# Kernel optimization log

Measured on AMD Instinct MI355X. Metric: run time of the kernel, lower is better.

Reference implementation:

```python
import jax, jax.numpy as jnp
import numpy as np

RADIUS = 1.0
BUMP = 32          # config.bump_steps
SCALE = 100.0      # sigmoid sharpness in compute_ecc
G = 32             # num_graphs

N, E, F = 16000, 48000, 32000
DIM, NDIR = 3, 64
HID, NC = 256, 10


def compute_ecc(h, index, lin):
    # h: [M, D]; lin: [BUMP] thresholds; index: [M] graph ids
    # sigmoid(scale * (lin - h)) broadcast -> [M, BUMP, D], segment-sum over M
    ecc = jax.nn.sigmoid(SCALE * (lin[None, :, None] - h[:, None, :]))
    return jax.ops.segment_sum(ecc, index, num_segments=G)  # [G, BUMP, D]


def setup_inputs() -> dict:
    key = jax.random.key(0)
    ks = jax.random.split(key, 12)
    x = jax.random.normal(ks[0], (N, DIM), dtype=jnp.float32)
    node_weights = jax.random.uniform(ks[1], (N,), dtype=jnp.float32)
    edge_weights = jax.random.uniform(ks[2], (E,), dtype=jnp.float32)
    face_weights = jax.random.uniform(ks[3], (F,), dtype=jnp.float32)
    v = jax.random.normal(ks[4], (DIM, NDIR), dtype=jnp.float32)
    v = v / jnp.linalg.norm(v, axis=0, keepdims=True)  # unit directions
    W1 = jax.random.normal(ks[5], (HID, NDIR * BUMP), dtype=jnp.float32) * 0.02
    b1 = jnp.zeros((HID,), dtype=jnp.float32)
    W2 = jax.random.normal(ks[6], (NC, HID), dtype=jnp.float32) * 0.02
    b2 = jnp.zeros((NC,), dtype=jnp.float32)
    edge_index = jax.random.randint(ks[7], (2, E), 0, N, dtype=jnp.int64)
    face = jax.random.randint(ks[8], (3, F), 0, N, dtype=jnp.int64)
    batch_ids = jnp.sort(jax.random.randint(ks[9], (N,), 0, G, dtype=jnp.int64))
    return {"x": x, "node_weights": node_weights, "edge_weights": edge_weights,
            "face_weights": face_weights, "v": v, "W1": W1, "b1": b1,
            "W2": W2, "b2": b2, "edge_index": edge_index, "face": face,
            "batch_ids": batch_ids}


def reference(x, node_weights, edge_weights, face_weights, v, W1, b1, W2, b2,
              edge_index, face, batch_ids):
    lin = jnp.linspace(-RADIUS, RADIUS, BUMP, dtype=jnp.float32)
    # node heights: weighted coords projected onto directions -> [N, D]
    nh = (x * node_weights[:, None]) @ v
    # edge heights: max over the 2 endpoints, then weight -> [E, D]
    eh = jnp.maximum(nh[edge_index[0]], nh[edge_index[1]]) * edge_weights[:, None]
    idx_e = batch_ids[edge_index[0]]
    # face heights: max over the 3 vertices -> [F, D]
    fh = jnp.max(nh[face], axis=0) * face_weights[:, None]
    idx_f = batch_ids[face[0]]
    ecc = compute_ecc(nh, batch_ids, lin)   # [G, BUMP, D]
    ecc = ecc - compute_ecc(eh, idx_e, lin)
    ecc = ecc + compute_ecc(fh, idx_f, lin)
    flat = ecc.reshape(G, -1)               # [G, BUMP*D]
    h = jax.nn.relu(flat @ W1.T + b1)
    logits = h @ W2.T + b2
    return (logits, flat)
```

## Files before the change

### kernel.cpp

```cpp
#include <hip/hip_runtime.h>
#include <hip/hip_bf16.h>

constexpr int NN = 16000, NE = 48000, NF = 32000;
constexpr int ND = 64, NB = 32, NG = 32;
constexpr int HIDN = 256, NCLS = 10;
constexpr int CHB = 32;
constexpr int EFB = (NE + NF + 255) / 256;
constexpr int PREB = (NN * 16) / 256;
constexpr int CAPE = 4096, CAPF = 4096;
constexpr float KLOG = 144.26950408889634f;
constexpr float DLT  = 9.307710457348151f;
constexpr float INV_DLT = 0.10743849569269015f;
constexpr int HBINS = 39;

struct alignas(8)  ERec { unsigned ab; float w; };
struct alignas(16) FRec { unsigned ab; unsigned c; float w; unsigned pad; };

constexpr int NH_OFF   = 0;
constexpr int ECCF_OFF = NH_OFF + NN * ND;
constexpr int CUR_OFF  = ECCF_OFF + NG * NB * ND;
constexpr int NOFS_OFF = CUR_OFF + 64;
constexpr int DONE_OFF = NOFS_OFF + 40;
constexpr int ER_OFF   = DONE_OFF + 32;
constexpr int FR_OFF   = ER_OFF + NG * CAPE * 2;
constexpr int HB_OFF   = FR_OFF + NG * CAPF * 4;
constexpr int ZERO_CNT = NG * NB * ND;

__device__ __forceinline__ int clamp_node(int n) {
    return ((unsigned)n < (unsigned)NN) ? n : 0;
}
template<bool BF> __device__ __forceinline__ float ldf(const void* p, int i) {
    return BF ? __bfloat162float(((const __hip_bfloat16*)p)[i]) : ((const float*)p)[i];
}
template<bool BF> __device__ __forceinline__ float4 ldf4(const void* p, int i) {
    if (BF) {
        uint2 u = *(const uint2*)((const unsigned short*)p + i);
        float4 r;
        r.x = __uint_as_float((u.x & 0xffffu) << 16);
        r.y = __uint_as_float(u.x & 0xffff0000u);
        r.z = __uint_as_float((u.y & 0xffffu) << 16);
        r.w = __uint_as_float(u.y & 0xffff0000u);
        return r;
    }
    return *(const float4*)((const float*)p + i);
}
template<bool I64> __device__ __forceinline__ int ldi(const int* p, int i) {
    return I64 ? p[2 * i] : p[i];
}

__device__ __forceinline__ bool detect_bf(const void* xp) {
    const unsigned* xw = (const unsigned*)xp;
    unsigned w = xw[threadIdx.x & 63];
    return __ballot(((w >> 23) & 0xFFu) >= 200u) != 0ull;
}
__device__ __forceinline__ bool detect_i64(const int* eip) {
    const unsigned* eiw = (const unsigned*)eip;
    unsigned o = eiw[2 * (threadIdx.x & 63) + 1];
    return __ballot(o != 0u) == 0ull;
}

__device__ __forceinline__ void accum_hist(float h, float s, float* hb) {
    const float KDEC = __builtin_amdgcn_exp2f(-DLT);
    float hkL = fmaf(h, KLOG, KLOG);
    float fl = floorf((hkL - 14.0f) * INV_DLT);
    int jlo = (int)fl + 1;
    if (jlo >= 32) return;
    if (jlo < -4) { hb[4 * 64] += s; return; }
    float t0 = fmaf(-(fl + 1.0f), DLT, hkL);
    float e  = __builtin_amdgcn_exp2f(t0);
    float s0 = __builtin_amdgcn_rcpf(1.0f + e);  e *= KDEC;
    float s1 = __builtin_amdgcn_rcpf(1.0f + e);  e *= KDEC;
    float s2 = __builtin_amdgcn_rcpf(1.0f + e);
    float* p = hb + (jlo + 4) * 64;
    float v0 = p[0], v1 = p[64], v2 = p[128], v3 = p[192];
    p[0]   = v0 + s * s0;
    p[64]  = v1 + s * (s1 - s0);
    p[128] = v2 + s * (s2 - s1);
    p[192] = v3 + s * (1.0f - s2);
}

template<bool BF, bool I64>
__device__ __forceinline__ void pre_body(const void* x, const void* nw, const void* v,
                                         const int* ei, const int* fc, const int* batch,
                                         const void* ew, const void* fw,
                                         float* wsf, int* wsi, unsigned* cur,
                                         ERec* er, FRec* fr,
                                         unsigned* cnt, unsigned* base) {
    int t = threadIdx.x;
    int gid = blockIdx.x * 256 + t;

    if (gid < ZERO_CNT / 4) {
        float4 z; z.x = z.y = z.z = z.w = 0.0f;
        *(float4*)(wsf + ECCF_OFF + gid * 4) = z;
    }

    if (blockIdx.x == PREB - 1 && t < 32)
        ((unsigned*)wsi)[DONE_OFF + t] = 0u;

    if (gid < NN) {
        int gn = ldi<I64>(batch, gid) & (NG - 1);
        int gp = (gid > 0) ? (ldi<I64>(batch, gid - 1) & (NG - 1)) : -1;
        for (int gg = gp + 1; gg <= gn; gg++) wsi[NOFS_OFF + gg] = gid;
        if (gid == NN - 1)
            for (int gg = gn + 1; gg <= NG; gg++) wsi[NOFS_OFF + gg] = NN;
    }

    {
        int n = gid >> 4, d0 = (gid & 15) * 4;
        float x0 = ldf<BF>(x, n * 3 + 0), x1 = ldf<BF>(x, n * 3 + 1);
        float x2 = ldf<BF>(x, n * 3 + 2), wn = ldf<BF>(nw, n);
        float4 v0 = ldf4<BF>(v, d0);
        float4 v1 = ldf4<BF>(v, ND + d0);
        float4 v2 = ldf4<BF>(v, 2 * ND + d0);
        float4 h;
        h.x = fmaf(x2, v2.x, fmaf(x1, v1.x, x0 * v0.x)) * wn;
        h.y = fmaf(x2, v2.y, fmaf(x1, v1.y, x0 * v0.y)) * wn;
        h.z = fmaf(x2, v2.z, fmaf(x1, v1.z, x0 * v0.z)) * wn;
        h.w = fmaf(x2, v2.w, fmaf(x1, v1.w, x0 * v0.w)) * wn;
        *(float4*)(wsf + NH_OFF + n * ND + d0) = h;
    }

    if (blockIdx.x < EFB) {
        if (t < 64) cnt[t] = 0;
        __syncthreads();
        int id = blockIdx.x * 256 + t;
        int bin = 0; unsigned rank = 0; bool act = false;
        if (id < NE + NF) {
            if (id < NE) bin = ldi<I64>(batch, clamp_node(ldi<I64>(ei, id))) & 31;
            else bin = 32 + (ldi<I64>(batch, clamp_node(ldi<I64>(fc, id - NE))) & 31);
            act = true;
            rank = atomicAdd(&cnt[bin], 1u);
        }
        __syncthreads();
        if (t < 64) base[t] = cnt[t] ? atomicAdd(&cur[t], cnt[t]) : 0u;
        __syncthreads();
        if (act) {
            int off = (int)(base[bin] + rank);
            if (bin < 32) {
                if (off < CAPE) {
                    unsigned a = (unsigned)clamp_node(ldi<I64>(ei, id));
                    unsigned b = (unsigned)clamp_node(ldi<I64>(ei, NE + id));
                    ERec r; r.ab = a | (b << 14); r.w = ldf<BF>(ew, id);
                    er[bin * CAPE + off] = r;
                }
            } else {
                if (off < CAPF) {
                    int fid = id - NE;
                    unsigned a = (unsigned)clamp_node(ldi<I64>(fc, fid));
                    unsigned b = (unsigned)clamp_node(ldi<I64>(fc, NF + fid));
                    unsigned c = (unsigned)clamp_node(ldi<I64>(fc, 2 * NF + fid));
                    FRec r; r.ab = a | (b << 14); r.c = c;
                    r.w = ldf<BF>(fw, fid); r.pad = 0u;
                    fr[(bin - 32) * CAPF + off] = r;
                }
            }
        }
    }
}
__global__ __launch_bounds__(256) void k_pre(const void* __restrict__ x,
                                             const void* __restrict__ nw,
                                             const void* __restrict__ v,
                                             const int* __restrict__ ei,
                                             const int* __restrict__ fc,
                                             const int* __restrict__ batch,
                                             const void* __restrict__ ew,
                                             const void* __restrict__ fw,
                                             float* __restrict__ wsf,
                                             int* __restrict__ wsi,
                                             unsigned* __restrict__ cur,
                                             ERec* __restrict__ er,
                                             FRec* __restrict__ fr) {
    __shared__ unsigned cnt[64], base[64];
    bool bf = detect_bf(x), i64 = detect_i64(ei);
    if (bf)  { if (i64) pre_body<true,true >(x,nw,v,ei,fc,batch,ew,fw,wsf,wsi,cur,er,fr,cnt,base);
               else     pre_body<true,false>(x,nw,v,ei,fc,batch,ew,fw,wsf,wsi,cur,er,fr,cnt,base); }
    else     { if (i64) pre_body<false,true >(x,nw,v,ei,fc,batch,ew,fw,wsf,wsi,cur,er,fr,cnt,base);
               else     pre_body<false,false>(x,nw,v,ei,fc,batch,ew,fw,wsf,wsi,cur,er,fr,cnt,base); }
}

__global__ __launch_bounds__(256, 4) void k_ecc(const float* __restrict__ nh,
                                                const int* __restrict__ wsi,
                                                const unsigned* __restrict__ cur,
                                                float* __restrict__ eccf,
                                                const ERec* __restrict__ er,
                                                const FRec* __restrict__ fr) {
    __shared__ float hist[4 * HBINS * 64];
    int t = threadIdx.x;
    int d = t & 63;
    int w = __builtin_amdgcn_readfirstlane(t) >> 6;
    int g  = blockIdx.x >> 5;
    int cb = blockIdx.x & (CHB - 1);
    int sid = cb * 4 + w;
    const int S = CHB * 4;

    for (int j = t; j < 4 * HBINS * 64; j += 256) hist[j] = 0.0f;
    __syncthreads();

    float* hb = hist + w * (HBINS * 64) + d;

    int ns = wsi[NOFS_OFF + g], nend = wsi[NOFS_OFF + g + 1];
    int i = ns + sid;
    for (; i + 3 * S < nend; i += 4 * S) {
        float h1 = nh[i * ND + d];
        float h2 = nh[(i + S) * ND + d];
        float h3 = nh[(i + 2 * S) * ND + d];
        float h4 = nh[(i + 3 * S) * ND + d];
        accum_hist(h1, 1.0f, hb);
        accum_hist(h2, 1.0f, hb);
        accum_hist(h3, 1.0f, hb);
        accum_hist(h4, 1.0f, hb);
    }
    for (; i < nend; i += S) accum_hist(nh[i * ND + d], 1.0f, hb);

    int ecnt = min((int)cur[g], CAPE);
    const ERec* eg = er + g * CAPE;
    i = sid;
    if (i + 3 * S < ecnt) {
        ERec r1 = eg[i], r2 = eg[i + S], r3 = eg[i + 2 * S], r4 = eg[i + 3 * S];
        for (;;) {
            int ni = i + 4 * S;
            bool more = (ni + 3 * S < ecnt);
            float a1 = nh[(r1.ab & 16383) * ND + d], b1 = nh[((r1.ab >> 14) & 16383) * ND + d];
            float a2 = nh[(r2.ab & 16383) * ND + d], b2 = nh[((r2.ab >> 14) & 16383) * ND + d];
            float a3 = nh[(r3.ab & 16383) * ND + d], b3 = nh[((r3.ab >> 14) & 16383) * ND + d];
            float a4 = nh[(r4.ab & 16383) * ND + d], b4 = nh[((r4.ab >> 14) & 16383) * ND + d];
            ERec n1, n2, n3, n4;
            if (more) { n1 = eg[ni]; n2 = eg[ni + S]; n3 = eg[ni + 2 * S]; n4 = eg[ni + 3 * S]; }
            accum_hist(fmaxf(a1, b1) * r1.w, -1.0f, hb);
            accum_hist(fmaxf(a2, b2) * r2.w, -1.0f, hb);
            accum_hist(fmaxf(a3, b3) * r3.w, -1.0f, hb);
            accum_hist(fmaxf(a4, b4) * r4.w, -1.0f, hb);
            i = ni;
            if (!more) break;
            r1 = n1; r2 = n2; r3 = n3; r4 = n4;
        }
    }
    for (; i < ecnt; i += S) {
        ERec r = eg[i];
        float ha = nh[(r.ab & 16383) * ND + d], hbv = nh[((r.ab >> 14) & 16383) * ND + d];
        accum_hist(fmaxf(ha, hbv) * r.w, -1.0f, hb);
    }

    int fcnt = min((int)cur[32 + g], CAPF);
    const FRec* fg = fr + g * CAPF;
    i = sid;
    if (i + 3 * S < fcnt) {
        FRec r1 = fg[i], r2 = fg[i + S], r3 = fg[i + 2 * S], r4 = fg[i + 3 * S];
        for (;;) {
            int ni = i + 4 * S;
            bool more = (ni + 3 * S < fcnt);
            float a1 = nh[(r1.ab & 16383) * ND + d], b1 = nh[((r1.ab >> 14) & 16383) * ND + d];
            float c1 = nh[r1.c * ND + d];
            float a2 = nh[(r2.ab & 16383) * ND + d], b2 = nh[((r2.ab >> 14) & 16383) * ND + d];
            float c2 = nh[r2.c * ND + d];
            float a3 = nh[(r3.ab & 16383) * ND + d], b3 = nh[((r3.ab >> 14) & 16383) * ND + d];
            float c3 = nh[r3.c * ND + d];
            float a4 = nh[(r4.ab & 16383) * ND + d], b4 = nh[((r4.ab >> 14) & 16383) * ND + d];
            float c4 = nh[r4.c * ND + d];
            FRec n1, n2, n3, n4;
            if (more) { n1 = fg[ni]; n2 = fg[ni + S]; n3 = fg[ni + 2 * S]; n4 = fg[ni + 3 * S]; }
            accum_hist(fmaxf(fmaxf(a1, b1), c1) * r1.w, 1.0f, hb);
            accum_hist(fmaxf(fmaxf(a2, b2), c2) * r2.w, 1.0f, hb);
            accum_hist(fmaxf(fmaxf(a3, b3), c3) * r3.w, 1.0f, hb);
            accum_hist(fmaxf(fmaxf(a4, b4), c4) * r4.w, 1.0f, hb);
            i = ni;
            if (!more) break;
            r1 = n1; r2 = n2; r3 = n3; r4 = n4;
        }
    }
    for (; i < fcnt; i += S) {
        FRec r = fg[i];
        float ha = nh[(r.ab & 16383) * ND + d], hbv = nh[((r.ab >> 14) & 16383) * ND + d];
        float hc = nh[r.c * ND + d];
        accum_hist(fmaxf(fmaxf(ha, hbv), hc) * r.w, 1.0f, hb);
    }

    __syncthreads();
    for (int o = t; o < HBINS * 64; o += 256)
        hist[o] += hist[HBINS*64 + o] + hist[2*HBINS*64 + o] + hist[3*HBINS*64 + o];
    __syncthreads();
    {
        float* segw = hist + HBINS * 64;
        float run = 0.0f, pre[8];
#pragma unroll
        for (int jj = 0; jj < 8; jj++) {
            run += hist[(4 + w * 8 + jj) * 64 + d];
            pre[jj] = run;
        }
        float padb = hist[d] + hist[64 + d] + hist[128 + d] + hist[192 + d];
        segw[w * 64 + d] = run;
        __syncthreads();
        float base = padb;
#pragma unroll
        for (int u = 0; u < 3; u++) if (u < w) base += segw[u * 64 + d];
        float* eb = eccf + g * (NB * ND) + d;
#pragma unroll
        for (int jj = 0; jj < 8; jj++)
            unsafeAtomicAdd(eb + (w * 8 + jj) * 64, base + pre[jj]);
    }
}

template<bool BF>
__device__ __forceinline__ void mlp_body(const void* W1, const void* b1,
                                         const void* W2, const void* b2,
                                         const float* eccf, float* hbuf,
                                         unsigned* done, void* outv,
                                         float* red, float* pr, unsigned* lastflag) {
    int g = blockIdx.x >> 3, hc = blockIdx.x & 7;
    int t = threadIdx.x;

    const float4* fp = (const float4*)(eccf + g * (NB * ND) + t * 8);
    float4 fa = fp[0], fb = fp[1];
    float fl[8] = {fa.x, fa.y, fa.z, fa.w, fb.x, fb.y, fb.z, fb.w};

    if (hc == 0) {
        int ob = NG * NCLS + g * (NB * ND) + t * 8;
        if (BF) {
#pragma unroll
            for (int j = 0; j < 8; j++)
                ((__hip_bfloat16*)outv)[ob + j] = __float2bfloat16(fl[j]);
        } else {
            ((float4*)((float*)outv + ob))[0] = fa;
            ((float4*)((float*)outv + ob))[1] = fb;
        }
    }

    float acc[32];
#pragma unroll
    for (int r = 0; r < 32; r++) acc[r] = 0.0f;
#pragma unroll 4
    for (int r = 0; r < 32; r++) {
        size_t wb = (size_t)(hc * 32 + r) * (NB * ND) + t * 8;
        float wv[8];
        if (BF) {
            uint4 u = *(const uint4*)((const __hip_bfloat16*)W1 + wb);
            wv[0] = __uint_as_float(u.x << 16); wv[1] = __uint_as_float(u.x & 0xffff0000u);
            wv[2] = __uint_as_float(u.y << 16); wv[3] = __uint_as_float(u.y & 0xffff0000u);
            wv[4] = __uint_as_float(u.z << 16); wv[5] = __uint_as_float(u.z & 0xffff0000u);
            wv[6] = __uint_as_float(u.w << 16); wv[7] = __uint_as_float(u.w & 0xffff0000u);
        } else {
            float4 a = *(const float4*)((const float*)W1 + wb);
            float4 b = *(const float4*)((const float*)W1 + wb + 4);
            wv[0]=a.x; wv[1]=a.y; wv[2]=a.z; wv[3]=a.w;
            wv[4]=b.x; wv[5]=b.y; wv[6]=b.z; wv[7]=b.w;
        }
        float s = 0.0f;
#pragma unroll
        for (int j = 0; j < 8; j++) s = fmaf(wv[j], fl[j], s);
        acc[r] = s;
    }

#pragma unroll
    for (int r = 0; r < 32; r++) red[t * 33 + r] = acc[r];
    __syncthreads();
    {
        int r = t >> 3, s8 = t & 7;
        float sum = 0.0f;
#pragma unroll
        for (int i = 0; i < 32; i++) sum += red[(s8 * 32 + i) * 33 + r];
        pr[r * 8 + s8] = sum;
    }
    __syncthreads();
    if (t < 32) {
        float h = ldf<BF>(b1, hc * 32 + t);
#pragma unroll
        for (int s8 = 0; s8 < 8; s8++) h += pr[t * 8 + s8];
        __hip_atomic_store(&hbuf[g * HIDN + hc * 32 + t], fmaxf(h, 0.0f),
                           __ATOMIC_RELAXED, __HIP_MEMORY_SCOPE_AGENT);
    }

    __syncthreads();
    if (t == 0) {
        unsigned prev = __hip_atomic_fetch_add(&done[g], 1u, __ATOMIC_RELAXED,
                                               __HIP_MEMORY_SCOPE_AGENT);
        *lastflag = (prev == 7u) ? 1u : 0u;
    }
    __syncthreads();
    if (*lastflag) {
        red[t] = __hip_atomic_load(&hbuf[g * HIDN + t], __ATOMIC_RELAXED,
                                   __HIP_MEMORY_SCOPE_AGENT);
        __syncthreads();
        int w = t >> 6, lane = t & 63;
        for (int c = w; c < NCLS; c += 4) {
            float p = red[lane]        * ldf<BF>(W2, c * HIDN + lane)
                    + red[lane + 64]   * ldf<BF>(W2, c * HIDN + lane + 64)
                    + red[lane + 128]  * ldf<BF>(W2, c * HIDN + lane + 128)
                    + red[lane + 192]  * ldf<BF>(W2, c * HIDN + lane + 192);
#pragma unroll
            for (int off = 32; off >= 1; off >>= 1) p += __shfl_xor(p, off);
            if (lane == 0) {
                float r = p + ldf<BF>(b2, c);
                if (BF) ((__hip_bfloat16*)outv)[g * NCLS + c] = __float2bfloat16(r);
                else    ((float*)outv)[g * NCLS + c] = r;
            }
        }
    }
}
__global__ __launch_bounds__(256) void k_mlp(const void* __restrict__ W1,
                                             const void* __restrict__ b1,
                                             const void* __restrict__ W2,
                                             const void* __restrict__ b2,
                                             const float* __restrict__ eccf,
                                             float* __restrict__ hbuf,
                                             unsigned* __restrict__ done,
                                             void* __restrict__ outv,
                                             const void* __restrict__ x) {
    __shared__ float red[256 * 33];
    __shared__ float pr[256];
    __shared__ unsigned lastflag;
    if (detect_bf(x)) mlp_body<true >(W1, b1, W2, b2, eccf, hbuf, done, outv, red, pr, &lastflag);
    else              mlp_body<false>(W1, b1, W2, b2, eccf, hbuf, done, outv, red, pr, &lastflag);
}

extern "C" void kernel_launch(void* const* d_in, const int* in_sizes, int n_in,
                              void* d_out, int out_size, void* d_ws, size_t ws_size,
                              hipStream_t stream) {
    const void* x  = d_in[0];
    const void* nw = d_in[1];
    const void* ew = d_in[2];
    const void* fw = d_in[3];
    const void* v  = d_in[4];
    const void* W1 = d_in[5];
    const void* b1 = d_in[6];
    const void* W2 = d_in[7];
    const void* b2 = d_in[8];
    const int* ei    = (const int*)d_in[9];
    const int* fc    = (const int*)d_in[10];
    const int* batch = (const int*)d_in[11];

    float*    wsf = (float*)d_ws;
    unsigned* wsu = (unsigned*)d_ws;
    int*      wsi = (int*)d_ws;
    float*    nh   = wsf + NH_OFF;
    float*    eccf = wsf + ECCF_OFF;
    unsigned* cur  = wsu + CUR_OFF;
    unsigned* done = wsu + DONE_OFF;
    float*    hbuf = wsf + HB_OFF;
    ERec*     er   = (ERec*)(wsf + ER_OFF);
    FRec*     fr   = (FRec*)(wsf + FR_OFF);

    hipMemsetAsync((char*)d_ws + (size_t)CUR_OFF * 4, 0, 64 * 4, stream);

    k_pre<<<PREB, 256, 0, stream>>>(x, nw, v, ei, fc, batch, ew, fw, wsf, wsi, cur, er, fr);
    k_ecc<<<NG * CHB, 256, 0, stream>>>(nh, wsi, cur, eccf, er, fr);
    k_mlp<<<NG * 8, 256, 0, stream>>>(W1, b1, W2, b2, eccf, hbuf, done, d_out, x);
}
```

Baseline: 120.9 us.

## Drop node-height buffer; prebake weighted vertex coords into edge/face records

Stops materialising the N×64 node-height array in the pre kernel. Edge and face records now carry the pre-weighted 3D coordinates of each endpoint plus the element weight, and the ecc kernel computes heights on the fly as a dot product with the direction vector held in registers. Node heights are likewise recomputed from x and the node weights. This replaces the scattered per-direction gathers from the 4 MB height buffer with contiguous float4 record loads. The cost is larger records (32 or 48 bytes each), more FMAs in the histogram loop, and a shallower unroll with no software prefetch.

```diff
diff --git a/kernel.cpp b/kernel.cpp
--- a/kernel.cpp
+++ b/kernel.cpp
@@ -6,24 +6,20 @@
 constexpr int HIDN = 256, NCLS = 10;
 constexpr int CHB = 32;
 constexpr int EFB = (NE + NF + 255) / 256;
-constexpr int PREB = (NN * 16) / 256;
+constexpr int PREB = EFB;
 constexpr int CAPE = 4096, CAPF = 4096;
 constexpr float KLOG = 144.26950408889634f;
 constexpr float DLT  = 9.307710457348151f;
 constexpr float INV_DLT = 0.10743849569269015f;
 constexpr int HBINS = 39;
 
-struct alignas(8)  ERec { unsigned ab; float w; };
-struct alignas(16) FRec { unsigned ab; unsigned c; float w; unsigned pad; };
-
-constexpr int NH_OFF   = 0;
-constexpr int ECCF_OFF = NH_OFF + NN * ND;
+constexpr int ECCF_OFF = 0;
 constexpr int CUR_OFF  = ECCF_OFF + NG * NB * ND;
 constexpr int NOFS_OFF = CUR_OFF + 64;
 constexpr int DONE_OFF = NOFS_OFF + 40;
 constexpr int ER_OFF   = DONE_OFF + 32;
-constexpr int FR_OFF   = ER_OFF + NG * CAPE * 2;
-constexpr int HB_OFF   = FR_OFF + NG * CAPF * 4;
+constexpr int FR_OFF   = ER_OFF + NG * CAPE * 8;
+constexpr int HB_OFF   = FR_OFF + NG * CAPF * 12;
 constexpr int ZERO_CNT = NG * NB * ND;
 
 __device__ __forceinline__ int clamp_node(int n) {
@@ -31,18 +27,6 @@
 }
 template<bool BF> __device__ __forceinline__ float ldf(const void* p, int i) {
     return BF ? __bfloat162float(((const __hip_bfloat16*)p)[i]) : ((const float*)p)[i];
-}
-template<bool BF> __device__ __forceinline__ float4 ldf4(const void* p, int i) {
-    if (BF) {
-        uint2 u = *(const uint2*)((const unsigned short*)p + i);
-        float4 r;
-        r.x = __uint_as_float((u.x & 0xffffu) << 16);
-        r.y = __uint_as_float(u.x & 0xffff0000u);
-        r.z = __uint_as_float((u.y & 0xffffu) << 16);
-        r.w = __uint_as_float(u.y & 0xffff0000u);
-        return r;
-    }
-    return *(const float4*)((const float*)p + i);
 }
 template<bool I64> __device__ __forceinline__ int ldi(const int* p, int i) {
     return I64 ? p[2 * i] : p[i];
@@ -57,6 +41,10 @@
     const unsigned* eiw = (const unsigned*)eip;
     unsigned o = eiw[2 * (threadIdx.x & 63) + 1];
     return __ballot(o != 0u) == 0ull;
+}
+
+__device__ __forceinline__ float dot3w(float4 p, float v0, float v1, float v2) {
+    return fmaf(p.z, v2, fmaf(p.y, v1, p.x * v0));
 }
 
 __device__ __forceinline__ void accum_hist(float h, float s, float* hb) {
@@ -80,11 +68,11 @@
 }
 
 template<bool BF, bool I64>
-__device__ __forceinline__ void pre_body(const void* x, const void* nw, const void* v,
+__device__ __forceinline__ void pre_body(const void* x, const void* nw,
                                          const int* ei, const int* fc, const int* batch,
                                          const void* ew, const void* fw,
                                          float* wsf, int* wsi, unsigned* cur,
-                                         ERec* er, FRec* fr,
+                                         float4* er4, float4* fr4,
                                          unsigned* cnt, unsigned* base) {
     int t = threadIdx.x;
     int gid = blockIdx.x * 256 + t;
@@ -94,7 +82,7 @@
         *(float4*)(wsf + ECCF_OFF + gid * 4) = z;
     }
 
-    if (blockIdx.x == PREB - 1 && t < 32)
+    if (blockIdx.x == 0 && t < 32)
         ((unsigned*)wsi)[DONE_OFF + t] = 0u;
 
     if (gid < NN) {
@@ -106,24 +94,9 @@
     }
 
     {
-        int n = gid >> 4, d0 = (gid & 15) * 4;
-        float x0 = ldf<BF>(x, n * 3 + 0), x1 = ldf<BF>(x, n * 3 + 1);
-        float x2 = ldf<BF>(x, n * 3 + 2), wn = ldf<BF>(nw, n);
-        float4 v0 = ldf4<BF>(v, d0);
-        float4 v1 = ldf4<BF>(v, ND + d0);
-        float4 v2 = ldf4<BF>(v, 2 * ND + d0);
-        float4 h;
-        h.x = fmaf(x2, v2.x, fmaf(x1, v1.x, x0 * v0.x)) * wn;
-        h.y = fmaf(x2, v2.y, fmaf(x1, v1.y, x0 * v0.y)) * wn;
-        h.z = fmaf(x2, v2.z, fmaf(x1, v1.z, x0 * v0.z)) * wn;
-        h.w = fmaf(x2, v2.w, fmaf(x1, v1.w, x0 * v0.w)) * wn;
-        *(float4*)(wsf + NH_OFF + n * ND + d0) = h;
-    }
-
-    if (blockIdx.x < EFB) {
         if (t < 64) cnt[t] = 0;
         __syncthreads();
-        int id = blockIdx.x * 256 + t;
+        int id = gid;
         int bin = 0; unsigned rank = 0; bool act = false;
         if (id < NE + NF) {
             if (id < NE) bin = ldi<I64>(batch, clamp_node(ldi<I64>(ei, id))) & 31;
@@ -138,20 +111,43 @@
             int off = (int)(base[bin] + rank);
             if (bin < 32) {
                 if (off < CAPE) {
-                    unsigned a = (unsigned)clamp_node(ldi<I64>(ei, id));
-                    unsigned b = (unsigned)clamp_node(ldi<I64>(ei, NE + id));
-                    ERec r; r.ab = a | (b << 14); r.w = ldf<BF>(ew, id);
-                    er[bin * CAPE + off] = r;
+                    int a = clamp_node(ldi<I64>(ei, id));
+                    int b = clamp_node(ldi<I64>(ei, NE + id));
+                    float wa = ldf<BF>(nw, a), wb = ldf<BF>(nw, b);
+                    float4 ra, rb;
+                    ra.x = ldf<BF>(x, 3*a)   * wa;
+                    ra.y = ldf<BF>(x, 3*a+1) * wa;
+                    ra.z = ldf<BF>(x, 3*a+2) * wa;
+                    ra.w = ldf<BF>(ew, id);
+                    rb.x = ldf<BF>(x, 3*b)   * wb;
+                    rb.y = ldf<BF>(x, 3*b+1) * wb;
+                    rb.z = ldf<BF>(x, 3*b+2) * wb;
+                    rb.w = 0.0f;
+                    float4* dst = er4 + ((size_t)bin * CAPE + off) * 2;
+                    dst[0] = ra; dst[1] = rb;
                 }
             } else {
                 if (off < CAPF) {
                     int fid = id - NE;
-                    unsigned a = (unsigned)clamp_node(ldi<I64>(fc, fid));
-                    unsigned b = (unsigned)clamp_node(ldi<I64>(fc, NF + fid));
-                    unsigned c = (unsigned)clamp_node(ldi<I64>(fc, 2 * NF + fid));
-                    FRec r; r.ab = a | (b << 14); r.c = c;
-                    r.w = ldf<BF>(fw, fid); r.pad = 0u;
-                    fr[(bin - 32) * CAPF + off] = r;
+                    int a = clamp_node(ldi<I64>(fc, fid));
+                    int b = clamp_node(ldi<I64>(fc, NF + fid));
+                    int c = clamp_node(ldi<I64>(fc, 2 * NF + fid));
+                    float wa = ldf<BF>(nw, a), wb = ldf<BF>(nw, b), wc = ldf<BF>(nw, c);
+                    float4 qa, qb, qc;
+                    qa.x = ldf<BF>(x, 3*a)   * wa;
+                    qa.y = ldf<BF>(x, 3*a+1) * wa;
+                    qa.z = ldf<BF>(x, 3*a+2) * wa;
+                    qa.w = ldf<BF>(fw, fid);
+                    qb.x = ldf<BF>(x, 3*b)   * wb;
+                    qb.y = ldf<BF>(x, 3*b+1) * wb;
+                    qb.z = ldf<BF>(x, 3*b+2) * wb;
+                    qb.w = 0.0f;
+                    qc.x = ldf<BF>(x, 3*c)   * wc;
+                    qc.y = ldf<BF>(x, 3*c+1) * wc;
+                    qc.z = ldf<BF>(x, 3*c+2) * wc;
+                    qc.w = 0.0f;
+                    float4* dst = fr4 + ((size_t)(bin - 32) * CAPF + off) * 3;
+                    dst[0] = qa; dst[1] = qb; dst[2] = qc;
                 }
             }
         }
@@ -159,7 +155,6 @@
 }
 __global__ __launch_bounds__(256) void k_pre(const void* __restrict__ x,
                                              const void* __restrict__ nw,
-                                             const void* __restrict__ v,
                                              const int* __restrict__ ei,
                                              const int* __restrict__ fc,
                                              const int* __restrict__ batch,
@@ -168,23 +163,21 @@
                                              float* __restrict__ wsf,
                                              int* __restrict__ wsi,
                                              unsigned* __restrict__ cur,
-                                             ERec* __restrict__ er,
-                                             FRec* __restrict__ fr) {
+                                             float4* __restrict__ er4,
+                                             float4* __restrict__ fr4) {
     __shared__ unsigned cnt[64], base[64];
     bool bf = detect_bf(x), i64 = detect_i64(ei);
-    if (bf)  { if (i64) pre_body<true,true >(x,nw,v,ei,fc,batch,ew,fw,wsf,wsi,cur,er,fr,cnt,base);
-               else     pre_body<true,false>(x,nw,v,ei,fc,batch,ew,fw,wsf,wsi,cur,er,fr,cnt,base); }
-    else     { if (i64) pre_body<false,true >(x,nw,v,ei,fc,batch,ew,fw,wsf,wsi,cur,er,fr,cnt,base);
-               else     pre_body<false,false>(x,nw,v,ei,fc,batch,ew,fw,wsf,wsi,cur,er,fr,cnt,base); }
-}
-
-__global__ __launch_bounds__(256, 4) void k_ecc(const float* __restrict__ nh,
-                                                const int* __restrict__ wsi,
-                                                const unsigned* __restrict__ cur,
-                                                float* __restrict__ eccf,
-                                                const ERec* __restrict__ er,
-                                                const FRec* __restrict__ fr) {
-    __shared__ float hist[4 * HBINS * 64];
+    if (bf)  { if (i64) pre_body<true,true >(x,nw,ei,fc,batch,ew,fw,wsf,wsi,cur,er4,fr4,cnt,base);
+               else     pre_body<true,false>(x,nw,ei,fc,batch,ew,fw,wsf,wsi,cur,er4,fr4,cnt,base); }
+    else     { if (i64) pre_body<false,true >(x,nw,ei,fc,batch,ew,fw,wsf,wsi,cur,er4,fr4,cnt,base);
+               else     pre_body<false,false>(x,nw,ei,fc,batch,ew,fw,wsf,wsi,cur,er4,fr4,cnt,base); }
+}
+
+template<bool BF>
+__device__ __forceinline__ void ecc_body(const void* xx, const void* nw, const void* vv,
+                                         const int* wsi, const unsigned* cur,
+                                         float* eccf, const float4* er4,
+                                         const float4* fr4, float* hist) {
     int t = threadIdx.x;
     int d = t & 63;
     int w = __builtin_amdgcn_readfirstlane(t) >> 6;
@@ -193,91 +186,76 @@
     int sid = cb * 4 + w;
     const int S = CHB * 4;
 
-    for (int j = t; j < 4 * HBINS * 64; j += 256) hist[j] = 0.0f;
+    float v0 = ldf<BF>(vv, d), v1 = ldf<BF>(vv, ND + d), v2 = ldf<BF>(vv, 2 * ND + d);
+
+    float4* h4 = (float4*)hist;
+    const int Q = HBINS * 16;
+    float4 z; z.x = z.y = z.z = z.w = 0.0f;
+    for (int j = t; j < 4 * Q; j += 256) h4[j] = z;
     __syncthreads();
 
     float* hb = hist + w * (HBINS * 64) + d;
 
     int ns = wsi[NOFS_OFF + g], nend = wsi[NOFS_OFF + g + 1];
     int i = ns + sid;
-    for (; i + 3 * S < nend; i += 4 * S) {
-        float h1 = nh[i * ND + d];
-        float h2 = nh[(i + S) * ND + d];
-        float h3 = nh[(i + 2 * S) * ND + d];
-        float h4 = nh[(i + 3 * S) * ND + d];
+    for (; i + S < nend; i += 2 * S) {
+        int j = i + S;
+        float a0 = ldf<BF>(xx, 3*i), a1 = ldf<BF>(xx, 3*i+1), a2 = ldf<BF>(xx, 3*i+2);
+        float wa = ldf<BF>(nw, i);
+        float b0 = ldf<BF>(xx, 3*j), b1 = ldf<BF>(xx, 3*j+1), b2 = ldf<BF>(xx, 3*j+2);
+        float wb = ldf<BF>(nw, j);
+        accum_hist(fmaf(a2, v2, fmaf(a1, v1, a0 * v0)) * wa, 1.0f, hb);
+        accum_hist(fmaf(b2, v2, fmaf(b1, v1, b0 * v0)) * wb, 1.0f, hb);
+    }
+    for (; i < nend; i += S) {
+        float a0 = ldf<BF>(xx, 3*i), a1 = ldf<BF>(xx, 3*i+1), a2 = ldf<BF>(xx, 3*i+2);
+        float wa = ldf<BF>(nw, i);
+        accum_hist(fmaf(a2, v2, fmaf(a1, v1, a0 * v0)) * wa, 1.0f, hb);
+    }
+
+    int ecnt = min((int)cur[g], CAPE);
+    const float4* eg = er4 + (size_t)g * CAPE * 2;
+    i = sid;
+    for (; i + S < ecnt; i += 2 * S) {
+        float4 pa1 = eg[2*i],       pb1 = eg[2*i + 1];
+        float4 pa2 = eg[2*(i+S)],   pb2 = eg[2*(i+S) + 1];
+        float h1 = fmaxf(dot3w(pa1, v0, v1, v2), dot3w(pb1, v0, v1, v2)) * pa1.w;
+        float h2 = fmaxf(dot3w(pa2, v0, v1, v2), dot3w(pb2, v0, v1, v2)) * pa2.w;
+        accum_hist(h1, -1.0f, hb);
+        accum_hist(h2, -1.0f, hb);
+    }
+    for (; i < ecnt; i += S) {
+        float4 pa = eg[2*i], pb = eg[2*i + 1];
+        accum_hist(fmaxf(dot3w(pa, v0, v1, v2), dot3w(pb, v0, v1, v2)) * pa.w,
+                   -1.0f, hb);
+    }
+
+    int fcnt = min((int)cur[32 + g], CAPF);
+    const float4* fg = fr4 + (size_t)g * CAPF * 3;
+    i = sid;
+    for (; i + S < fcnt; i += 2 * S) {
+        float4 qa1 = fg[3*i], qb1 = fg[3*i + 1], qc1 = fg[3*i + 2];
+        float4 qa2 = fg[3*(i+S)], qb2 = fg[3*(i+S) + 1], qc2 = fg[3*(i+S) + 2];
+        float h1 = fmaxf(fmaxf(dot3w(qa1, v0, v1, v2), dot3w(qb1, v0, v1, v2)),
+                         dot3w(qc1, v0, v1, v2)) * qa1.w;
+        float h2 = fmaxf(fmaxf(dot3w(qa2, v0, v1, v2), dot3w(qb2, v0, v1, v2)),
+                         dot3w(qc2, v0, v1, v2)) * qa2.w;
         accum_hist(h1, 1.0f, hb);
         accum_hist(h2, 1.0f, hb);
-        accum_hist(h3, 1.0f, hb);
-        accum_hist(h4, 1.0f, hb);
-    }
-    for (; i < nend; i += S) accum_hist(nh[i * ND + d], 1.0f, hb);
-
-    int ecnt = min((int)cur[g], CAPE);
-    const ERec* eg = er + g * CAPE;
-    i = sid;
-    if (i + 3 * S < ecnt) {
-        ERec r1 = eg[i], r2 = eg[i + S], r3 = eg[i + 2 * S], r4 = eg[i + 3 * S];
-        for (;;) {
-            int ni = i + 4 * S;
-            bool more = (ni + 3 * S < ecnt);
-            float a1 = nh[(r1.ab & 16383) * ND + d], b1 = nh[((r1.ab >> 14) & 16383) * ND + d];
-            float a2 = nh[(r2.ab & 16383) * ND + d], b2 = nh[((r2.ab >> 14) & 16383) * ND + d];
-            float a3 = nh[(r3.ab & 16383) * ND + d], b3 = nh[((r3.ab >> 14) & 16383) * ND + d];
-            float a4 = nh[(r4.ab & 16383) * ND + d], b4 = nh[((r4.ab >> 14) & 16383) * ND + d];
-            ERec n1, n2, n3, n4;
-            if (more) { n1 = eg[ni]; n2 = eg[ni + S]; n3 = eg[ni + 2 * S]; n4 = eg[ni + 3 * S]; }
-            accum_hist(fmaxf(a1, b1) * r1.w, -1.0f, hb);
-            accum_hist(fmaxf(a2, b2) * r2.w, -1.0f, hb);
-            accum_hist(fmaxf(a3, b3) * r3.w, -1.0f, hb);
-            accum_hist(fmaxf(a4, b4) * r4.w, -1.0f, hb);
-            i = ni;
-            if (!more) break;
-            r1 = n1; r2 = n2; r3 = n3; r4 = n4;
-        }
-    }
-    for (; i < ecnt; i += S) {
-        ERec r = eg[i];
-        float ha = nh[(r.ab & 16383) * ND + d], hbv = nh[((r.ab >> 14) & 16383) * ND + d];
-        accum_hist(fmaxf(ha, hbv) * r.w, -1.0f, hb);
-    }
-
-    int fcnt = min((int)cur[32 + g], CAPF);
-    const FRec* fg = fr + g * CAPF;
-    i = sid;
-    if (i + 3 * S < fcnt) {
-        FRec r1 = fg[i], r2 = fg[i + S], r3 = fg[i + 2 * S], r4 = fg[i + 3 * S];
-        for (;;) {
-            int ni = i + 4 * S;
-            bool more = (ni + 3 * S < fcnt);
-            float a1 = nh[(r1.ab & 16383) * ND + d], b1 = nh[((r1.ab >> 14) & 16383) * ND + d];
-            float c1 = nh[r1.c * ND + d];
-            float a2 = nh[(r2.ab & 16383) * ND + d], b2 = nh[((r2.ab >> 14) & 16383) * ND + d];
-            float c2 = nh[r2.c * ND + d];
-            float a3 = nh[(r3.ab & 16383) * ND + d], b3 = nh[((r3.ab >> 14) & 16383) * ND + d];
-            float c3 = nh[r3.c * ND + d];
-            float a4 = nh[(r4.ab & 16383) * ND + d], b4 = nh[((r4.ab >> 14) & 16383) * ND + d];
-            float c4 = nh[r4.c * ND + d];
-            FRec n1, n2, n3, n4;
-            if (more) { n1 = fg[ni]; n2 = fg[ni + S]; n3 = fg[ni + 2 * S]; n4 = fg[ni + 3 * S]; }
-            accum_hist(fmaxf(fmaxf(a1, b1), c1) * r1.w, 1.0f, hb);
-            accum_hist(fmaxf(fmaxf(a2, b2), c2) * r2.w, 1.0f, hb);
-            accum_hist(fmaxf(fmaxf(a3, b3), c3) * r3.w, 1.0f, hb);
-            accum_hist(fmaxf(fmaxf(a4, b4), c4) * r4.w, 1.0f, hb);
-            i = ni;
-            if (!more) break;
-            r1 = n1; r2 = n2; r3 = n3; r4 = n4;
-        }
     }
     for (; i < fcnt; i += S) {
-        FRec r = fg[i];
-        float ha = nh[(r.ab & 16383) * ND + d], hbv = nh[((r.ab >> 14) & 16383) * ND + d];
-        float hc = nh[r.c * ND + d];
-        accum_hist(fmaxf(fmaxf(ha, hbv), hc) * r.w, 1.0f, hb);
-    }
-
-    __syncthreads();
-    for (int o = t; o < HBINS * 64; o += 256)
-        hist[o] += hist[HBINS*64 + o] + hist[2*HBINS*64 + o] + hist[3*HBINS*64 + o];
+        float4 qa = fg[3*i], qb = fg[3*i + 1], qc = fg[3*i + 2];
+        accum_hist(fmaxf(fmaxf(dot3w(qa, v0, v1, v2), dot3w(qb, v0, v1, v2)),
+                         dot3w(qc, v0, v1, v2)) * qa.w, 1.0f, hb);
+    }
+
+    __syncthreads();
+    for (int o = t; o < Q; o += 256) {
+        float4 A = h4[o], B = h4[Q + o], C = h4[2*Q + o], D = h4[3*Q + o];
+        A.x += B.x + C.x + D.x;  A.y += B.y + C.y + D.y;
+        A.z += B.z + C.z + D.z;  A.w += B.w + C.w + D.w;
+        h4[o] = A;
+    }
     __syncthreads();
     {
         float* segw = hist + HBINS * 64;
@@ -298,6 +276,18 @@
         for (int jj = 0; jj < 8; jj++)
             unsafeAtomicAdd(eb + (w * 8 + jj) * 64, base + pre[jj]);
     }
+}
+__global__ __launch_bounds__(256, 4) void k_ecc(const void* __restrict__ x,
+                                                const void* __restrict__ nw,
+                                                const void* __restrict__ v,
+                                                const int* __restrict__ wsi,
+                                                const unsigned* __restrict__ cur,
+                                                float* __restrict__ eccf,
+                                                const float4* __restrict__ er4,
+                                                const float4* __restrict__ fr4) {
+    __shared__ float hist[4 * HBINS * 64];
+    if (detect_bf(x)) ecc_body<true >(x, nw, v, wsi, cur, eccf, er4, fr4, hist);
+    else              ecc_body<false>(x, nw, v, wsi, cur, eccf, er4, fr4, hist);
 }
 
 template<bool BF>
@@ -431,17 +421,16 @@
     float*    wsf = (float*)d_ws;
     unsigned* wsu = (unsigned*)d_ws;
     int*      wsi = (int*)d_ws;
-    float*    nh   = wsf + NH_OFF;
     float*    eccf = wsf + ECCF_OFF;
     unsigned* cur  = wsu + CUR_OFF;
     unsigned* done = wsu + DONE_OFF;
     float*    hbuf = wsf + HB_OFF;
-    ERec*     er   = (ERec*)(wsf + ER_OFF);
-    FRec*     fr   = (FRec*)(wsf + FR_OFF);
+    float4*   er4  = (float4*)(wsf + ER_OFF);
+    float4*   fr4  = (float4*)(wsf + FR_OFF);
 
     hipMemsetAsync((char*)d_ws + (size_t)CUR_OFF * 4, 0, 64 * 4, stream);
 
-    k_pre<<<PREB, 256, 0, stream>>>(x, nw, v, ei, fc, batch, ew, fw, wsf, wsi, cur, er, fr);
-    k_ecc<<<NG * CHB, 256, 0, stream>>>(nh, wsi, cur, eccf, er, fr);
+    k_pre<<<PREB, 256, 0, stream>>>(x, nw, ei, fc, batch, ew, fw, wsf, wsi, cur, er4, fr4);
+    k_ecc<<<NG * CHB, 256, 0, stream>>>(x, nw, v, wsi, cur, eccf, er4, fr4);
     k_mlp<<<NG * 8, 256, 0, stream>>>(W1, b1, W2, b2, eccf, hbuf, done, d_out, x);
 }
```

Result: no change. 118.6 us (-1.9%).
